# Optimization experiments

Hardware: AMD Instinct MI355X
Metric: run time of the kernel (lower is better)

The kernel has to match this reference:

```python
import jax, jax.numpy as jnp
import numpy as np

B, NV, NS, L = 32, 2048, 512, 64
FEAT, SEM, HID, ATT, DM = 1024, 512, 512, 512, 512


def setup_inputs() -> dict:
    key = jax.random.key(0)
    ks = jax.random.split(key, 14)
    s = lambda k, sh: jax.random.normal(k, sh, dtype=jnp.float32) * 0.02
    return {
        "query": jax.random.normal(ks[0], (B, 1, HID), dtype=jnp.float32),
        "visual_features": jax.random.normal(ks[1], (B, NV, FEAT), dtype=jnp.float32),
        "semantic_features": jax.random.normal(ks[2], (B, NS, SEM), dtype=jnp.float32),
        "patient_info": jax.random.normal(ks[3], (B, L, DM), dtype=jnp.float32),
        "W1v": s(ks[4], (HID, ATT)),
        "W2v": s(ks[5], (FEAT, ATT)),
        "vv": s(ks[6], (ATT, 1)),
        "W3": s(ks[7], (DM, ATT)),
        "b3": jnp.zeros((ATT,), dtype=jnp.float32),
        "W1s": s(ks[8], (HID, ATT)),
        "W2s": s(ks[9], (SEM, ATT)),
        "vs": s(ks[10], (ATT, 1)),
        "W": s(ks[11], (FEAT + SEM, FEAT)),
        "bW": jnp.zeros((FEAT,), dtype=jnp.float32),
    }


def reference(query, visual_features, semantic_features, patient_info,
              W1v, W2v, vv, W3, b3, W1s, W2s, vs, W, bW):
    # mean over patient sequence, project: [B,1,ATT]
    pinfo = jnp.mean(patient_info, axis=1, keepdims=True) @ W3 + b3
    q_v = query @ W1v          # [B,1,ATT]
    # visual branch
    v_scores = jnp.tanh(q_v + visual_features @ W2v + pinfo) @ vv  # [B,NV,1]
    v_attn = jax.nn.softmax(v_scores, axis=1)
    # semantic branch
    q_s = query @ W1s
    s_scores = jnp.tanh(q_s + semantic_features @ W2s + pinfo) @ vs  # [B,NS,1]
    s_attn = jax.nn.softmax(s_scores, axis=1)
    ctx = jnp.concatenate([
        jnp.sum(visual_features * v_attn, axis=1),    # [B,FEAT]
        jnp.sum(semantic_features * s_attn, axis=1),  # [B,SEM]
    ], axis=1) @ W + bW
    return ctx, v_attn, s_attn
```

## Files before the change

### kernel.cpp

```cpp
#include <hip/hip_runtime.h>

typedef float f32x4 __attribute__((ext_vector_type(4)));
typedef short short8 __attribute__((ext_vector_type(8)));

#define B_    32
#define NV_   2048
#define NS_   512
#define L_    64
#define FEAT_ 1024
#define SEM_  512
#define HID_  512
#define ATT_  512
#define DM_   512

#define FENCE asm volatile("" ::: "memory")

__device__ __forceinline__ unsigned int f2bf_pk(float lo, float hi) {
  unsigned int ul = (__float_as_uint(lo) + 0x8000u) >> 16;
  unsigned int uh = (__float_as_uint(hi) + 0x8000u) & 0xffff0000u;
  return uh | ul;
}

__device__ __forceinline__ unsigned short f2bf(float f) {
  return (unsigned short)((__float_as_uint(f) + 0x8000u) >> 16);
}

__device__ __forceinline__ float fast_tanh(float x) {
  float e = __expf(2.f * x);
  return 1.f - 2.f * __builtin_amdgcn_rcpf(e + 1.f);
}

__device__ __forceinline__ void gload16(const void* g, void* l) {
  __builtin_amdgcn_global_load_lds(
      (const __attribute__((address_space(1))) unsigned char*)g,
      (__attribute__((address_space(3))) unsigned char*)l, 16, 0, 0);
}

__global__ __launch_bounds__(256) void k_qp(const float* __restrict__ query,
                                            const float* __restrict__ pat,
                                            const float* __restrict__ W1v,
                                            const float* __restrict__ W1s,
                                            const float* __restrict__ W3,
                                            const float* __restrict__ b3,
                                            float* __restrict__ qpv,
                                            float* __restrict__ qps) {
  __shared__ float pmL[DM_];
  const int t = threadIdx.x;
  const int b = blockIdx.x >> 1;
  for (int d = t; d < DM_; d += 256) {
    float s = 0.f;
    for (int l = 0; l < L_; ++l) s += pat[(b * L_ + l) * DM_ + d];
    pmL[d] = s * (1.f / 64.f);
  }
  __syncthreads();
  const int a = (blockIdx.x & 1) * 256 + t;
  float pi = b3[a];
  for (int d = 0; d < DM_; ++d) pi += pmL[d] * W3[d * ATT_ + a];
  float qv = 0.f, qs = 0.f;
  for (int h = 0; h < HID_; ++h) {
    float q = query[b * HID_ + h];
    qv += q * W1v[h * ATT_ + a];
    qs += q * W1s[h * ATT_ + a];
  }
  qpv[b * ATT_ + a] = qv + pi;
  qps[b * ATT_ + a] = qs + pi;
}

__global__ __launch_bounds__(256) void k_swz2(const float* __restrict__ W2v,
                                              const float* __restrict__ W2s,
                                              unsigned short* __restrict__ outV,
                                              unsigned short* __restrict__ outS) {
  int idx = blockIdx.x * 256 + threadIdx.x;
  const float* src;
  unsigned short* dst;
  if (idx < FEAT_ * ATT_) {
    src = W2v; dst = outV;
  } else {
    idx -= FEAT_ * ATT_;
    if (idx >= SEM_ * ATT_) return;
    src = W2s; dst = outS;
  }
  int k = idx >> 9, c = idx & 511;
  int kc = k >> 5, kr = k & 31, q = kr >> 3, j = kr & 7;
  int cb = c >> 4, n = c & 15;
  dst[(kc * 32 + cb) * 512 + q * 128 + n * 8 + j] = f2bf(src[idx]);
}

__global__ __launch_bounds__(256, 2) void k_scores_fused(
    const float* __restrict__ X, const unsigned short* __restrict__ Wt,
    const float* __restrict__ qp, const float* __restrict__ vvec,
    float* __restrict__ score, int K, int rows_per_batch) {
  __shared__ __align__(16) char LdsA[2 * 4096];
  __shared__ __align__(16) char LdsB[2 * 32768];
  const int t = threadIdx.x;
  const int lane = t & 63, wave = t >> 6;
  const int quad = lane >> 4, l15 = lane & 15;
  const int row0 = blockIdx.x * 64;
  const int b = row0 / rows_per_batch;
  const int nk = K >> 5;

  const int r = t >> 2, q_ = t & 3;
  const float* gA = X + (size_t)(row0 + r) * K + q_ * 8;
  const int awOff = (r >> 4) * 1024 + q_ * 256 + (((r & 15) ^ (q_ << 1)) << 4);
  const int arOff = quad * 256 + ((l15 ^ (quad << 1)) << 4);
  const char* gBsrc = (const char*)Wt + (size_t)wave * 8192 + lane * 16;
  const int brOff = wave * 8192 + lane * 16;

  const f32x4 zero = {0.f, 0.f, 0.f, 0.f};
  f32x4 acc[4][8];
#pragma unroll
  for (int a = 0; a < 4; ++a)
#pragma unroll
    for (int cb = 0; cb < 8; ++cb) acc[a][cb] = zero;

  f32x4 T0a = *(const f32x4*)(gA);
  f32x4 T0b = *(const f32x4*)(gA + 4);
  FENCE;
  {
    char* dst = LdsB + wave * 8192;
#pragma unroll
    for (int i = 0; i < 8; ++i) gload16(gBsrc + i * 1024, dst + i * 1024);
  }
  FENCE;
  f32x4 A1a = *(const f32x4*)(gA + 32),  A1b = *(const f32x4*)(gA + 36);
  f32x4 A2a = *(const f32x4*)(gA + 64),  A2b = *(const f32x4*)(gA + 68);
  f32x4 A3a = *(const f32x4*)(gA + 96),  A3b = *(const f32x4*)(gA + 100);
  f32x4 A0a = *(const f32x4*)(gA + 128), A0b = *(const f32x4*)(gA + 132);
  FENCE;
  {
    uint4 w;
    w.x = f2bf_pk(T0a.x, T0a.y); w.y = f2bf_pk(T0a.z, T0a.w);
    w.z = f2bf_pk(T0b.x, T0b.y); w.w = f2bf_pk(T0b.z, T0b.w);
    *(uint4*)(LdsA + awOff) = w;
  }
  asm volatile("s_waitcnt lgkmcnt(0)\n\ts_waitcnt vmcnt(8)" ::: "memory");
  __builtin_amdgcn_s_barrier();
  FENCE;

#define STEP(KC, Pa, Pb)                                                       \
  {                                                                            \
    const int kc = (KC);                                                       \
    \
    uint4 w;                                                                   \
    w.x = f2bf_pk(Pa.x, Pa.y); w.y = f2bf_pk(Pa.z, Pa.w);                      \
    w.z = f2bf_pk(Pb.x, Pb.y); w.w = f2bf_pk(Pb.z, Pb.w);                      \
    *(uint4*)(LdsA + ((kc + 1) & 1) * 4096 + awOff) = w;                       \
    FENCE;                                                                     \
        \
    {                                                                          \
      const int kn = (kc + 1 < nk) ? kc + 1 : nk - 1;                          \
      const char* src = gBsrc + (size_t)kn * 32768;                            \
      char* dst = LdsB + ((kc + 1) & 1) * 32768 + wave * 8192;                 \
      _Pragma("unroll")                                                        \
      for (int i = 0; i < 8; ++i) gload16(src + i * 1024, dst + i * 1024);     \
    }                                                                          \
    FENCE;                                                                     \
                    \
    {                                                                          \
      const int kn5 = (kc + 5 < nk) ? kc + 5 : nk - 1;                         \
      Pa = *(const f32x4*)(gA + (size_t)kn5 * 32);                             \
      Pb = *(const f32x4*)(gA + (size_t)kn5 * 32 + 4);                         \
    }                                                                          \
    FENCE;                                                                     \
       \
    asm volatile("s_waitcnt lgkmcnt(0)\n\ts_waitcnt vmcnt(12)" ::: "memory");  \
    __builtin_amdgcn_s_barrier();                                              \
    FENCE;                                                                     \
                                    \
    {                                                                          \
      const char* ab = LdsA + (kc & 1) * 4096;                                 \
      const char* bb = LdsB + (kc & 1) * 32768;                                \
      short8 af[4], bf8[8];                                                    \
      _Pragma("unroll")                                                        \
      for (int a = 0; a < 4; ++a) af[a] = *(const short8*)(ab + a * 1024 + arOff); \
      _Pragma("unroll")                                                        \
      for (int j = 0; j < 8; ++j) bf8[j] = *(const short8*)(bb + brOff + j * 1024); \
      __builtin_amdgcn_s_setprio(1);                                           \
      _Pragma("unroll")                                                        \
      for (int a = 0; a < 4; ++a)                                              \
        _Pragma("unroll")                                                      \
        for (int j = 0; j < 8; ++j)                                            \
          acc[a][j] = __builtin_amdgcn_mfma_f32_16x16x32_bf16(af[a], bf8[j], acc[a][j], 0, 0, 0); \
      __builtin_amdgcn_s_setprio(0);                                           \
    }                                                                          \
    FENCE;                                                                     \
    __builtin_amdgcn_s_barrier(); \
    FENCE;                                                                     \
  }

  for (int kb = 0; kb < nk; kb += 4) {
    STEP(kb + 0, A1a, A1b);
    STEP(kb + 1, A2a, A2b);
    STEP(kb + 2, A3a, A3b);
    STEP(kb + 3, A0a, A0b);
  }
#undef STEP

  float qv_[8], vw_[8];
#pragma unroll
  for (int cb = 0; cb < 8; ++cb) {
    int col = wave * 128 + cb * 16 + l15;
    qv_[cb] = qp[b * ATT_ + col];
    vw_[cb] = vvec[col];
  }
#pragma unroll
  for (int a = 0; a < 4; ++a) {
#pragma unroll
    for (int rr = 0; rr < 4; ++rr) {
      float s = 0.f;
#pragma unroll
      for (int cb = 0; cb < 8; ++cb)
        s += fast_tanh(acc[a][cb][rr] + qv_[cb]) * vw_[cb];
      s += __shfl_xor(s, 1);
      s += __shfl_xor(s, 2);
      s += __shfl_xor(s, 4);
      s += __shfl_xor(s, 8);
      if (l15 == 0) atomicAdd(&score[row0 + a * 16 + quad * 4 + rr], s);
    }
  }
}

__global__ __launch_bounds__(256) void k_softmax2(const float* __restrict__ scores_v,
                                                  const float* __restrict__ scores_s,
                                                  float* __restrict__ v_attn,
                                                  float* __restrict__ s_attn) {
  __shared__ float sm[4];
  const int bb = blockIdx.x, t = threadIdx.x;
  const float* s;
  float* dst;
  int N;
  if (bb < 32) { s = scores_v + (size_t)bb * NV_; dst = v_attn + (size_t)bb * NV_; N = NV_; }
  else         { s = scores_s + (size_t)(bb - 32) * NS_; dst = s_attn + (size_t)(bb - 32) * NS_; N = NS_; }
  float m = -1e30f;
  for (int i = t; i < N; i += 256) m = fmaxf(m, s[i]);
  for (int k = 32; k; k >>= 1) m = fmaxf(m, __shfl_xor(m, k));
  if ((t & 63) == 0) sm[t >> 6] = m;
  __syncthreads();
  m = fmaxf(fmaxf(sm[0], sm[1]), fmaxf(sm[2], sm[3]));
  __syncthreads();
  float sum = 0.f;
  for (int i = t; i < N; i += 256) sum += __expf(s[i] - m);
  for (int k = 32; k; k >>= 1) sum += __shfl_xor(sum, k);
  if ((t & 63) == 0) sm[t >> 6] = sum;
  __syncthreads();
  sum = sm[0] + sm[1] + sm[2] + sm[3];
  float inv = 1.f / sum;
  for (int i = t; i < N; i += 256) dst[i] = __expf(s[i] - m) * inv;
}

__global__ __launch_bounds__(256) void k_wsum2(const float* __restrict__ vf,
                                               const float* __restrict__ sf,
                                               const float* __restrict__ v_attn,
                                               const float* __restrict__ s_attn,
                                               float* __restrict__ ctx_pre) {
  const int b = blockIdx.x, y = blockIdx.y, t = threadIdx.x;
  const float* feats;
  const float* attn;
  int N, F, colOff, r0;
  if (y < 8) { feats = vf; attn = v_attn; N = NV_; F = FEAT_; colOff = 0;     r0 = y * 256; }
  else       { feats = sf; attn = s_attn; N = NS_; F = SEM_;  colOff = 1024;  r0 = (y - 8) * 256; }
  const int c4 = t * 4;
  if (c4 >= F) return;
  const float* fb = feats + ((size_t)b * N + r0) * F;
  const float* ab = attn + (size_t)b * N + r0;
  float4 acc = {0.f, 0.f, 0.f, 0.f};
#pragma unroll 4
  for (int r = 0; r < 256; ++r) {
    float a = ab[r];
    float4 v = *(const float4*)(fb + (size_t)r * F + c4);
    acc.x += a * v.x; acc.y += a * v.y; acc.z += a * v.z; acc.w += a * v.w;
  }
  float* dst = ctx_pre + b * 1536 + colOff + c4;
  atomicAdd(dst + 0, acc.x);
  atomicAdd(dst + 1, acc.y);
  atomicAdd(dst + 2, acc.z);
  atomicAdd(dst + 3, acc.w);
}

__global__ __launch_bounds__(256) void k_final(const float* __restrict__ cp,
                                               const float* __restrict__ W,
                                               const float* __restrict__ bW,
                                               float* __restrict__ out) {
  int b = blockIdx.x, oc = blockIdx.y, t = threadIdx.x;
  int o = oc * 256 + t;
  float acc = bW[o];
  const float* c = cp + b * 1536;
  for (int k = 0; k < 1536; ++k) acc += c[k] * W[k * FEAT_ + o];
  out[b * FEAT_ + o] = acc;
}

extern "C" void kernel_launch(void* const* d_in, const int* in_sizes, int n_in,
                              void* d_out, int out_size, void* d_ws, size_t ws_size,
                              hipStream_t stream) {
  const float* query = (const float*)d_in[0];
  const float* vf    = (const float*)d_in[1];
  const float* sf    = (const float*)d_in[2];
  const float* pat   = (const float*)d_in[3];
  const float* W1v   = (const float*)d_in[4];
  const float* W2v   = (const float*)d_in[5];
  const float* vv    = (const float*)d_in[6];
  const float* W3    = (const float*)d_in[7];
  const float* b3    = (const float*)d_in[8];
  const float* W1s   = (const float*)d_in[9];
  const float* W2s   = (const float*)d_in[10];
  const float* vs    = (const float*)d_in[11];
  const float* W     = (const float*)d_in[12];
  const float* bW    = (const float*)d_in[13];
  float* out = (float*)d_out;

  char* ws = (char*)d_ws;
  float* scores_v = (float*)(ws);
  float* scores_s = (float*)(ws + 262144);
  float* ctx_pre  = (float*)(ws + 327680);
  float* qpv      = (float*)(ws + 524288);
  float* qps      = (float*)(ws + 589824);
  unsigned short* Wtv = (unsigned short*)(ws + 655360);
  unsigned short* Wts = (unsigned short*)(ws + 655360 + 1048576);

  hipMemsetAsync(d_ws, 0, 524288, stream);

  k_swz2<<<(FEAT_ * ATT_ + SEM_ * ATT_) / 256, 256, 0, stream>>>(W2v, W2s, Wtv, Wts);
  k_qp<<<64, 256, 0, stream>>>(query, pat, W1v, W1s, W3, b3, qpv, qps);

  float* v_attn = out + B_ * FEAT_;
  float* s_attn = out + B_ * FEAT_ + B_ * NV_;

  k_scores_fused<<<(B_ * NV_) / 64, 256, 0, stream>>>(vf, Wtv, qpv, vv, scores_v, FEAT_, NV_);
  k_scores_fused<<<(B_ * NS_) / 64, 256, 0, stream>>>(sf, Wts, qps, vs, scores_s, SEM_, NS_);
  k_softmax2<<<64, 256, 0, stream>>>(scores_v, scores_s, v_attn, s_attn);
  k_wsum2<<<dim3(B_, 10), 256, 0, stream>>>(vf, sf, v_attn, s_attn, ctx_pre);
  k_final<<<dim3(B_, 4), 256, 0, stream>>>(ctx_pre, W, bW, out);
}
```

Measured before the change: 664.9 us.

## Merge score launches and widen grids for qp and weighted-sum kernels

Measured after the change: 633.7 us. 4.7% less time.

```diff
diff --git a/kernel.cpp b/kernel.cpp
--- a/kernel.cpp
+++ b/kernel.cpp
@@ -45,25 +45,37 @@
                                             float* __restrict__ qpv,
                                             float* __restrict__ qps) {
   __shared__ float pmL[DM_];
+  __shared__ float red[3][4][64];
   const int t = threadIdx.x;
-  const int b = blockIdx.x >> 1;
+  const int b = blockIdx.x >> 3, aq = blockIdx.x & 7;
   for (int d = t; d < DM_; d += 256) {
     float s = 0.f;
     for (int l = 0; l < L_; ++l) s += pat[(b * L_ + l) * DM_ + d];
     pmL[d] = s * (1.f / 64.f);
   }
   __syncthreads();
-  const int a = (blockIdx.x & 1) * 256 + t;
-  float pi = b3[a];
-  for (int d = 0; d < DM_; ++d) pi += pmL[d] * W3[d * ATT_ + a];
-  float qv = 0.f, qs = 0.f;
-  for (int h = 0; h < HID_; ++h) {
+  const int al = t & 63, seg = t >> 6;
+  const int a = aq * 64 + al;
+  const int d0 = seg * 128;
+  float pi = 0.f, qv = 0.f, qs = 0.f;
+  for (int d = d0; d < d0 + 128; ++d) pi += pmL[d] * W3[d * ATT_ + a];
+  for (int h = d0; h < d0 + 128; ++h) {
     float q = query[b * HID_ + h];
     qv += q * W1v[h * ATT_ + a];
     qs += q * W1s[h * ATT_ + a];
   }
-  qpv[b * ATT_ + a] = qv + pi;
-  qps[b * ATT_ + a] = qs + pi;
+  red[0][seg][al] = pi;
+  red[1][seg][al] = qv;
+  red[2][seg][al] = qs;
+  __syncthreads();
+  if (t < 64) {
+    const int ao = aq * 64 + t;
+    float p = red[0][0][t] + red[0][1][t] + red[0][2][t] + red[0][3][t] + b3[ao];
+    float v = red[1][0][t] + red[1][1][t] + red[1][2][t] + red[1][3][t];
+    float s = red[2][0][t] + red[2][1][t] + red[2][2][t] + red[2][3][t];
+    qpv[b * ATT_ + ao] = v + p;
+    qps[b * ATT_ + ao] = s + p;
+  }
 }
 
 __global__ __launch_bounds__(256) void k_swz2(const float* __restrict__ W2v,
@@ -86,16 +98,34 @@
   dst[(kc * 32 + cb) * 512 + q * 128 + n * 8 + j] = f2bf(src[idx]);
 }
 
-__global__ __launch_bounds__(256, 2) void k_scores_fused(
-    const float* __restrict__ X, const unsigned short* __restrict__ Wt,
-    const float* __restrict__ qp, const float* __restrict__ vvec,
-    float* __restrict__ score, int K, int rows_per_batch) {
+__global__ __launch_bounds__(256, 2) void k_scores2(
+    const float* __restrict__ vf, const float* __restrict__ sf,
+    const unsigned short* __restrict__ Wtv, const unsigned short* __restrict__ Wts,
+    const float* __restrict__ qpv, const float* __restrict__ qps,
+    const float* __restrict__ vv, const float* __restrict__ vs,
+    float* __restrict__ scores_v, float* __restrict__ scores_s) {
   __shared__ __align__(16) char LdsA[2 * 4096];
   __shared__ __align__(16) char LdsB[2 * 32768];
+  const float* X;
+  const unsigned short* Wt;
+  const float* qp;
+  const float* vvec;
+  float* score;
+  int K, rows_per_batch, row0;
+  {
+    int bid = blockIdx.x;
+    if (bid < (B_ * NV_) / 64) {
+      X = vf; Wt = Wtv; qp = qpv; vvec = vv; score = scores_v;
+      K = FEAT_; rows_per_batch = NV_; row0 = bid * 64;
+    } else {
+      bid -= (B_ * NV_) / 64;
+      X = sf; Wt = Wts; qp = qps; vvec = vs; score = scores_s;
+      K = SEM_; rows_per_batch = NS_; row0 = bid * 64;
+    }
+  }
   const int t = threadIdx.x;
   const int lane = t & 63, wave = t >> 6;
   const int quad = lane >> 4, l15 = lane & 15;
-  const int row0 = blockIdx.x * 64;
   const int b = row0 / rows_per_batch;
   const int nk = K >> 5;
 
@@ -140,13 +170,11 @@
 #define STEP(KC, Pa, Pb)                                                       \
   {                                                                            \
     const int kc = (KC);                                                       \
-    \
     uint4 w;                                                                   \
     w.x = f2bf_pk(Pa.x, Pa.y); w.y = f2bf_pk(Pa.z, Pa.w);                      \
     w.z = f2bf_pk(Pb.x, Pb.y); w.w = f2bf_pk(Pb.z, Pb.w);                      \
     *(uint4*)(LdsA + ((kc + 1) & 1) * 4096 + awOff) = w;                       \
     FENCE;                                                                     \
-        \
     {                                                                          \
       const int kn = (kc + 1 < nk) ? kc + 1 : nk - 1;                          \
       const char* src = gBsrc + (size_t)kn * 32768;                            \
@@ -155,18 +183,15 @@
       for (int i = 0; i < 8; ++i) gload16(src + i * 1024, dst + i * 1024);     \
     }                                                                          \
     FENCE;                                                                     \
-                    \
     {                                                                          \
       const int kn5 = (kc + 5 < nk) ? kc + 5 : nk - 1;                         \
       Pa = *(const f32x4*)(gA + (size_t)kn5 * 32);                             \
       Pb = *(const f32x4*)(gA + (size_t)kn5 * 32 + 4);                         \
     }                                                                          \
     FENCE;                                                                     \
-       \
     asm volatile("s_waitcnt lgkmcnt(0)\n\ts_waitcnt vmcnt(12)" ::: "memory");  \
     __builtin_amdgcn_s_barrier();                                              \
     FENCE;                                                                     \
-                                    \
     {                                                                          \
       const char* ab = LdsA + (kc & 1) * 4096;                                 \
       const char* bb = LdsB + (kc & 1) * 32768;                                \
@@ -184,7 +209,7 @@
       __builtin_amdgcn_s_setprio(0);                                           \
     }                                                                          \
     FENCE;                                                                     \
-    __builtin_amdgcn_s_barrier(); \
+    __builtin_amdgcn_s_barrier();                                              \
     FENCE;                                                                     \
   }
 
@@ -254,18 +279,22 @@
                                                const float* __restrict__ s_attn,
                                                float* __restrict__ ctx_pre) {
   const int b = blockIdx.x, y = blockIdx.y, t = threadIdx.x;
-  const float* feats;
-  const float* attn;
-  int N, F, colOff, r0;
-  if (y < 8) { feats = vf; attn = v_attn; N = NV_; F = FEAT_; colOff = 0;     r0 = y * 256; }
-  else       { feats = sf; attn = s_attn; N = NS_; F = SEM_;  colOff = 1024;  r0 = (y - 8) * 256; }
-  const int c4 = t * 4;
-  if (c4 >= F) return;
-  const float* fb = feats + ((size_t)b * N + r0) * F;
-  const float* ab = attn + (size_t)b * N + r0;
+  const float* fb;
+  const float* ab;
+  int c4, colOff, rbeg, rend, F;
+  if (y < 32) {
+    const int r0 = y * 64;
+    fb = vf + ((size_t)b * NV_ + r0) * FEAT_;
+    ab = v_attn + (size_t)b * NV_ + r0;
+    F = FEAT_; colOff = 0; c4 = t * 4; rbeg = 0; rend = 64;
+  } else {
+    const int r0 = (y - 32) * 64;
+    fb = sf + ((size_t)b * NS_ + r0) * SEM_;
+    ab = s_attn + (size_t)b * NS_ + r0;
+    F = SEM_; colOff = 1024; c4 = (t & 127) * 4; rbeg = (t >> 7) * 32; rend = rbeg + 32;
+  }
   float4 acc = {0.f, 0.f, 0.f, 0.f};
-#pragma unroll 4
-  for (int r = 0; r < 256; ++r) {
+  for (int r = rbeg; r < rend; ++r) {
     float a = ab[r];
     float4 v = *(const float4*)(fb + (size_t)r * F + c4);
     acc.x += a * v.x; acc.y += a * v.y; acc.z += a * v.z; acc.w += a * v.w;
@@ -320,14 +349,14 @@
   hipMemsetAsync(d_ws, 0, 524288, stream);
 
   k_swz2<<<(FEAT_ * ATT_ + SEM_ * ATT_) / 256, 256, 0, stream>>>(W2v, W2s, Wtv, Wts);
-  k_qp<<<64, 256, 0, stream>>>(query, pat, W1v, W1s, W3, b3, qpv, qps);
+  k_qp<<<256, 256, 0, stream>>>(query, pat, W1v, W1s, W3, b3, qpv, qps);
 
   float* v_attn = out + B_ * FEAT_;
   float* s_attn = out + B_ * FEAT_ + B_ * NV_;
 
-  k_scores_fused<<<(B_ * NV_) / 64, 256, 0, stream>>>(vf, Wtv, qpv, vv, scores_v, FEAT_, NV_);
-  k_scores_fused<<<(B_ * NS_) / 64, 256, 0, stream>>>(sf, Wts, qps, vs, scores_s, SEM_, NS_);
+  k_scores2<<<(B_ * NV_) / 64 + (B_ * NS_) / 64, 256, 0, stream>>>(
+      vf, sf, Wtv, Wts, qpv, qps, vv, vs, scores_v, scores_s);
   k_softmax2<<<64, 256, 0, stream>>>(scores_v, scores_s, v_attn, s_attn);
-  k_wsum2<<<dim3(B_, 10), 256, 0, stream>>>(vf, sf, v_attn, s_attn, ctx_pre);
+  k_wsum2<<<dim3(B_, 40), 256, 0, stream>>>(vf, sf, v_attn, s_attn, ctx_pre);
   k_final<<<dim3(B_, 4), 256, 0, stream>>>(ctx_pre, W, bW, out);
 }
```
